# Performance work log

Measured on AMD Instinct MI355X. Metric: run time of the kernel, lower is better.

## Reference

```python
import jax, jax.numpy as jnp
import numpy as np

B, T, D, H, E = 16, 4096, 256, 512, 8


def setup_inputs() -> dict:
    key = jax.random.key(0)
    ks = jax.random.split(key, 5)
    x = jax.random.normal(ks[0], (B, T, D), dtype=jnp.float32)
    gate_w = jax.random.normal(ks[1], (D, E), dtype=jnp.float32) * 0.02
    gate_b = jnp.zeros((E,), dtype=jnp.float32)
    W1 = jax.random.normal(ks[2], (E, D, H), dtype=jnp.float32) * 0.02
    b1 = jnp.zeros((E, H), dtype=jnp.float32)
    W2 = jax.random.normal(ks[3], (E, H, D), dtype=jnp.float32) * 0.02
    b2 = jnp.zeros((E, D), dtype=jnp.float32)
    return {"x": x, "gate_w": gate_w, "gate_b": gate_b,
            "W1": W1, "b1": b1, "W2": W2, "b2": b2}


def reference(x, gate_w, gate_b, W1, b1, W2, b2):
    Bb, Tt, Dd = x.shape
    Ee = gate_w.shape[1]
    xf = x.reshape(-1, Dd)                       # [N, D]
    N = xf.shape[0]
    logits = xf @ gate_w + gate_b                # [N, E]
    probs = jax.nn.softmax(logits, axis=-1)
    top2_vals, top2_idx = jax.lax.top_k(probs, 2)  # [N, 2]
    # combine weights: w[n, e] = sum_k top2_vals[n,k] * (top2_idx[n,k]==e)
    cw = jnp.zeros((N, Ee), dtype=xf.dtype).at[
        jnp.arange(N)[:, None], top2_idx].add(top2_vals)  # [N, E]

    def step(acc, params):
        w1, bb1, w2, bb2, we = params            # per-expert slices
        h = jax.nn.gelu(xf @ w1 + bb1, approximate=False)  # [N, H]
        y = h @ w2 + bb2                          # [N, D]
        return acc + we[:, None] * y, None

    out, _ = jax.lax.scan(step, jnp.zeros_like(xf),
                          (W1, b1, W2, b2, cw.T))
    return out.reshape(Bb, Tt, Dd)
```

## Files before the change

### kernel.cpp

```cpp
#include <hip/hip_runtime.h>
#include <hip/hip_bf16.h>
#include <math.h>


#define N_TOK 65536
#define D_DIM 256
#define H_DIM 512
#define TILE_R 64
#define GRID_TILES 1088

typedef __bf16 bf16x8 __attribute__((ext_vector_type(8)));
typedef float f32x4 __attribute__((ext_vector_type(4)));

static __device__ __forceinline__ ushort f2bf(float f) {
    __hip_bfloat16 h = __float2bfloat16(f);
    ushort u;
    __builtin_memcpy(&u, &h, 2);
    return u;
}

static __device__ __forceinline__ float gelu(float v) {
    const float a = fabsf(v) * 0.70710678118654752f;
    const float t = __builtin_amdgcn_rcpf(fmaf(a, 0.47047f, 1.0f));
    const float p = t * fmaf(t, fmaf(t, 0.7478556f, -0.0958798f), 0.3480242f);
    const float er = fmaf(-p, __expf(-a * a), 1.0f);
    const float s = copysignf(er, v);
    return 0.5f * v * (1.0f + s);
}

__global__ __launch_bounds__(256) void prep(const float* __restrict__ x,
                                            const float* __restrict__ gate_w,
                                            const float* __restrict__ gate_b,
                                            const float* __restrict__ W1,
                                            const float* __restrict__ W2,
                                            ushort* __restrict__ xb,
                                            ushort* __restrict__ W1p,
                                            ushort* __restrict__ W2p,
                                            int* __restrict__ counts,
                                            int* __restrict__ pid_arr,
                                            float2* __restrict__ pw_arr) {
    __shared__ float gws[2048];
    __shared__ int lc[64];

    const int bid = blockIdx.x;
    const int tid = threadIdx.x;

    if (bid >= 2048) {
        const int pid = bid - 2048;
        const int t = (pid & 511) * 256 + tid;
        const int l = t & 63;
        const int lo = l & 15, hi = l >> 4;
        ushort v[8];
        if (pid < 512) {
            const int kb = (t >> 6) & 7;
            const int nb = (t >> 9) & 31;
            const int e  = t >> 14;
            const int k0 = kb * 32 + hi * 8;
            const int n  = nb * 16 + lo;
            const float* src = W1 + (size_t)e * D_DIM * H_DIM + n;
            #pragma unroll
            for (int j = 0; j < 8; ++j)
                v[j] = f2bf(src[(size_t)(k0 + j) * H_DIM]);
            *(uint4*)(W1p + (size_t)t * 8) = *(const uint4*)v;
        } else {
            const int kb = (t >> 6) & 15;
            const int nb = (t >> 10) & 15;
            const int e  = t >> 14;
            const int k0 = kb * 32 + hi * 8;
            const int n  = nb * 16 + lo;
            const float* src = W2 + (size_t)e * H_DIM * D_DIM + n;
            #pragma unroll
            for (int j = 0; j < 8; ++j)
                v[j] = f2bf(src[(size_t)(k0 + j) * D_DIM]);
            *(uint4*)(W2p + (size_t)t * 8) = *(const uint4*)v;
        }
        return;
    }

    const size_t t0 = (size_t)bid * 32;
    for (int i = tid; i < 2048; i += 256) gws[i] = gate_w[i];
    if (tid < 64) lc[tid] = 0;
    __syncthreads();

    const int m = tid >> 3, q = tid & 7;
    const float4* xr = (const float4*)(x + (t0 + m) * D_DIM + q * 32);
    ushort4* xw = (ushort4*)(xb + (t0 + m) * D_DIM + q * 32);

    double lg[8] = {0, 0, 0, 0, 0, 0, 0, 0};
    #pragma unroll
    for (int it = 0; it < 8; ++it) {
        const float4 v = xr[it];
        ushort4 bv;
        bv.x = f2bf(v.x); bv.y = f2bf(v.y); bv.z = f2bf(v.z); bv.w = f2bf(v.w);
        xw[it] = bv;
        const float* g = &gws[(q * 32 + it * 4) * 8];
        const float vv[4] = {v.x, v.y, v.z, v.w};
        #pragma unroll
        for (int j = 0; j < 4; ++j) {
            const double xv = (double)vv[j];
            #pragma unroll
            for (int e2 = 0; e2 < 8; ++e2) lg[e2] += xv * (double)g[j * 8 + e2];
        }
    }
    #pragma unroll
    for (int e2 = 0; e2 < 8; ++e2) {
        lg[e2] += __shfl_xor(lg[e2], 1, 64);
        lg[e2] += __shfl_xor(lg[e2], 2, 64);
        lg[e2] += __shfl_xor(lg[e2], 4, 64);
    }

    if (q == 0) {
        int e0 = 0, e1 = -1;
        #pragma unroll
        for (int e2 = 0; e2 < 8; ++e2) lg[e2] += (double)gate_b[e2];
        double b0 = -1e300, b1v = -1e300;
        #pragma unroll
        for (int e2 = 0; e2 < 8; ++e2)
            if (lg[e2] > b0) { b0 = lg[e2]; e0 = e2; }
        #pragma unroll
        for (int e2 = 0; e2 < 8; ++e2)
            if (e2 != e0 && lg[e2] > b1v) { b1v = lg[e2]; e1 = e2; }
        double s = 0;
        #pragma unroll
        for (int e2 = 0; e2 < 8; ++e2) s += exp(lg[e2] - b0);
        const float p0 = (float)(1.0 / s);
        const float p1 = (float)(exp(b1v - b0) / s);
        const int pid = e0 * 8 + e1;
        atomicAdd(&lc[pid], 1);
        const int tok = (int)t0 + m;
        pid_arr[tok] = pid;
        pw_arr[tok] = make_float2(p0, p1);
    }
    __syncthreads();
    if (tid < 64 && lc[tid]) atomicAdd(&counts[tid], lc[tid]);
}

__global__ __launch_bounds__(256) void scatter(const int* __restrict__ counts,
                                               const int* __restrict__ pid_arr,
                                               const float2* __restrict__ pw_arr,
                                               int* __restrict__ cursor,
                                               int* __restrict__ tok_list,
                                               float* __restrict__ w0l,
                                               float* __restrict__ w1l) {
    __shared__ int lcnt[64];
    __shared__ int lbase[64];
    const int tid = threadIdx.x;
    const int t = blockIdx.x * 256 + tid;
    if (tid < 64) lcnt[tid] = 0;
    __syncthreads();
    const int pid = pid_arr[t];
    const float2 pw = pw_arr[t];
    const int lpos = atomicAdd(&lcnt[pid], 1);
    __syncthreads();
    if (tid < 64) {
        int s = 0;
        for (int i = 0; i < tid; ++i) s += counts[i];
        const int mine = lcnt[tid];
        lbase[tid] = s + (mine ? atomicAdd(&cursor[tid], mine) : 0);
    }
    __syncthreads();
    const int pos = lbase[pid] + lpos;
    tok_list[pos] = t;
    w0l[pos] = pw.x;
    w1l[pos] = pw.y;
}

__global__ __launch_bounds__(512, 4) void moe_expert(const ushort* __restrict__ xb,
                                                     const ushort* __restrict__ W1p,
                                                     const ushort* __restrict__ W2p,
                                                     const float* __restrict__ b1,
                                                     const float* __restrict__ b2,
                                                     const int* __restrict__ counts,
                                                     const int* __restrict__ tok_list,
                                                     const float* __restrict__ w0l,
                                                     const float* __restrict__ w1l,
                                                     float* __restrict__ out) {
    __shared__ __align__(16) char Xs[TILE_R * 512];
    __shared__ __align__(16) char Hs[TILE_R * 512];
    __shared__ int   toks[TILE_R];
    __shared__ float wgt[2][TILE_R];

    int n = 0;
    for (int i = 0; i < 64; ++i) n += (counts[i] + 63) >> 6;
    const int qn = n >> 3, rn = n & 7;
    const int xc = blockIdx.x & 7, ix = blockIdx.x >> 3;
    if (ix >= qn + (xc < rn ? 1 : 0)) return;
    const int wg = xc * qn + min(xc, rn) + ix;

    int pid = -1, row0 = 0, nv = 0, gbase = 0;
    int st = 0, sc = 0;
    for (int i = 0; i < 64; ++i) {
        const int c = counts[i];
        const int nt = (c + 63) >> 6;
        if (pid < 0 && wg < st + nt) { pid = i; row0 = (wg - st) << 6; nv = min(TILE_R, c - row0); gbase = sc; }
        st += nt; sc += c;
    }
    const int ea = pid >> 3, eb = pid & 7;
    const int gidx = gbase + row0;

    const int tid = threadIdx.x;
    const int w = tid >> 6, l = tid & 63;
    const int lo = l & 15, hi = l >> 4;

    if (tid < TILE_R) {
        const bool vld = tid < nv;
        const int src = gidx + (vld ? tid : 0);
        toks[tid]   = tok_list[src];
        wgt[0][tid] = vld ? w0l[src] : 0.f;
        wgt[1][tid] = vld ? w1l[src] : 0.f;
    }

    {
        const int r = tid >> 3;
        const int tk = tok_list[gidx + min(r, nv - 1)];
        const char* src = (const char*)(xb + (size_t)tk * D_DIM) + (tid & 7) * 64;
        char* dst = Xs + r * 512;
        const int bo = (tid & 7) * 64, sw = (r & 7) << 4;
        #pragma unroll
        for (int c = 0; c < 4; ++c)
            *(uint4*)(dst + ((bo + c * 16) ^ sw)) = *(const uint4*)(src + c * 16);
    }
    __syncthreads();

    f32x4 acc2[4][2];
    #pragma unroll
    for (int mi = 0; mi < 4; ++mi)
        #pragma unroll
        for (int ni = 0; ni < 2; ++ni)
            acc2[mi][ni] = (f32x4){0.f, 0.f, 0.f, 0.f};

    #pragma unroll 1
    for (int phase = 0; phase < 4; ++phase) {
        const int ph = phase >> 1, ch = phase & 1;
        const int ew = ph ? eb : ea;

        const char* w1b = (const char*)W1p + (size_t)(ew * 32 + ch * 16 + w * 2) * 8192 + (size_t)l * 16;

        f32x4 acc1[2][4];
        #pragma unroll
        for (int nb = 0; nb < 2; ++nb)
            #pragma unroll
            for (int tb = 0; tb < 4; ++tb)
                acc1[nb][tb] = (f32x4){0.f, 0.f, 0.f, 0.f};

        bf16x8 wf[2][2];
        wf[0][0] = *(const bf16x8*)(w1b);
        wf[0][1] = *(const bf16x8*)(w1b + 8192);

        #pragma unroll
        for (int ks = 0; ks < 8; ++ks) {
            const int cb = ks & 1, nx = cb ^ 1;
            if (ks < 7) {
                wf[nx][0] = *(const bf16x8*)(w1b + (ks + 1) * 1024);
                wf[nx][1] = *(const bf16x8*)(w1b + 8192 + (ks + 1) * 1024);
            }
            #pragma unroll
            for (int tb = 0; tb < 4; ++tb) {
                const int slot = tb * 16 + lo;
                const bf16x8 xf = *(const bf16x8*)(Xs + slot * 512 +
                                  ((ks * 64 + hi * 16) ^ ((slot & 7) << 4)));
                __builtin_amdgcn_s_setprio(1);
                #pragma unroll
                for (int nb = 0; nb < 2; ++nb)
                    acc1[nb][tb] = __builtin_amdgcn_mfma_f32_16x16x32_bf16(wf[cb][nb], xf, acc1[nb][tb], 0, 0, 0);
                __builtin_amdgcn_s_setprio(0);
            }
        }

        #pragma unroll
        for (int nb = 0; nb < 2; ++nb) {
            const int hcE = (ch * 16 + w * 2 + nb) * 16 + hi * 4;
            const int hcH = (w * 2 + nb) * 16 + hi * 4;
            const float4 b1q = *(const float4*)(b1 + ew * H_DIM + hcE);
            #pragma unroll
            for (int tb = 0; tb < 4; ++tb) {
                const int slot = tb * 16 + lo;
                const float wt = wgt[ph][slot];
                ushort4 hv;
                hv.x = f2bf(gelu(acc1[nb][tb][0] + b1q.x) * wt);
                hv.y = f2bf(gelu(acc1[nb][tb][1] + b1q.y) * wt);
                hv.z = f2bf(gelu(acc1[nb][tb][2] + b1q.z) * wt);
                hv.w = f2bf(gelu(acc1[nb][tb][3] + b1q.w) * wt);
                *(ushort4*)(Hs + slot * 512 + ((hcH * 2) ^ ((slot & 7) << 4))) = hv;
            }
        }
        __syncthreads();

        const char* w2b = (const char*)W2p + ((size_t)(ew * 16 + w * 2) * 16 + ch * 8) * 1024 + (size_t)l * 16;

        bf16x8 wf2[3][2];
        #pragma unroll
        for (int p = 0; p < 2; ++p) {
            wf2[p][0] = *(const bf16x8*)(w2b + p * 1024);
            wf2[p][1] = *(const bf16x8*)(w2b + 16384 + p * 1024);
        }

        #pragma unroll
        for (int ks = 0; ks < 8; ++ks) {
            const int cb = ks % 3;
            if (ks < 6) {
                const int lb = (ks + 2) % 3;
                wf2[lb][0] = *(const bf16x8*)(w2b + (ks + 2) * 1024);
                wf2[lb][1] = *(const bf16x8*)(w2b + 16384 + (ks + 2) * 1024);
            }
            #pragma unroll
            for (int mi = 0; mi < 4; ++mi) {
                const int slot = mi * 16 + lo;
                const bf16x8 hf = *(const bf16x8*)(Hs + slot * 512 +
                                  ((ks * 64 + hi * 16) ^ ((slot & 7) << 4)));
                __builtin_amdgcn_s_setprio(1);
                #pragma unroll
                for (int ni = 0; ni < 2; ++ni)
                    acc2[mi][ni] = __builtin_amdgcn_mfma_f32_16x16x32_bf16(hf, wf2[cb][ni], acc2[mi][ni], 0, 0, 0);
                __builtin_amdgcn_s_setprio(0);
            }
        }
        if (phase < 3) __syncthreads();
    }

    #pragma unroll
    for (int ni = 0; ni < 2; ++ni) {
        const int col = w * 32 + ni * 16 + lo;
        const float b2a = b2[ea * D_DIM + col];
        const float b2b = b2[eb * D_DIM + col];
        #pragma unroll
        for (int mi = 0; mi < 4; ++mi) {
            #pragma unroll
            for (int rg = 0; rg < 4; ++rg) {
                const int r = mi * 16 + hi * 4 + rg;
                if (r < nv) {
                    const float v = acc2[mi][ni][rg] + wgt[0][r] * b2a + wgt[1][r] * b2b;
                    out[(size_t)toks[r] * D_DIM + col] = v;
                }
            }
        }
    }
}

extern "C" void kernel_launch(void* const* d_in, const int* in_sizes, int n_in,
                              void* d_out, int out_size, void* d_ws, size_t ws_size,
                              hipStream_t stream) {
    const float* x      = (const float*)d_in[0];
    const float* gate_w = (const float*)d_in[1];
    const float* gate_b = (const float*)d_in[2];
    const float* W1     = (const float*)d_in[3];
    const float* b1     = (const float*)d_in[4];
    const float* W2     = (const float*)d_in[5];
    const float* b2     = (const float*)d_in[6];
    float* out = (float*)d_out;

    char* ws = (char*)d_ws;
    ushort* xb      = (ushort*)(ws);
    ushort* W1p     = (ushort*)(ws + 33554432);
    ushort* W2p     = (ushort*)(ws + 35651584);
    int*    pid_arr = (int*)   (ws + 37748736);
    float2* pw_arr  = (float2*)(ws + 38010880);
    int*    tok_lst = (int*)   (ws + 38535168);
    float*  w0l     = (float*) (ws + 38797312);
    float*  w1l     = (float*) (ws + 39059456);
    int*    counts  = (int*)   (ws + 39321600);
    int*    cursor  = (int*)   (ws + 39321856);

    hipMemsetAsync(counts, 0, 512, stream);

    prep<<<dim3(3072), 256, 0, stream>>>(x, gate_w, gate_b, W1, W2,
                                         xb, W1p, W2p, counts, pid_arr, pw_arr);
    scatter<<<dim3(256), 256, 0, stream>>>(counts, pid_arr, pw_arr, cursor,
                                           tok_lst, w0l, w1l);
    moe_expert<<<dim3(GRID_TILES), 512, 0, stream>>>(xb, W1p, W2p, b1, b2, counts,
                                                     tok_lst, w0l, w1l, out);
}
```

Baseline: 199.9 us.

## Prefetch W1 fragments across phases with triple buffering and transpose gate weights

After: 185.7 us. 1.08x faster.

```diff
diff --git a/kernel.cpp b/kernel.cpp
--- a/kernel.cpp
+++ b/kernel.cpp
@@ -39,7 +39,7 @@
                                             int* __restrict__ counts,
                                             int* __restrict__ pid_arr,
                                             float2* __restrict__ pw_arr) {
-    __shared__ float gws[2048];
+    __shared__ float gwsT[8 * 260];
     __shared__ int lc[64];
 
     const int bid = blockIdx.x;
@@ -78,28 +78,32 @@
     }
 
     const size_t t0 = (size_t)bid * 32;
-    for (int i = tid; i < 2048; i += 256) gws[i] = gate_w[i];
+    for (int i = tid; i < 2048; i += 256) {
+        const int d = i >> 3, e = i & 7;
+        gwsT[e * 260 + d] = gate_w[i];
+    }
     if (tid < 64) lc[tid] = 0;
     __syncthreads();
 
     const int m = tid >> 3, q = tid & 7;
-    const float4* xr = (const float4*)(x + (t0 + m) * D_DIM + q * 32);
-    ushort4* xw = (ushort4*)(xb + (t0 + m) * D_DIM + q * 32);
+    const float* xrow = x + (t0 + m) * D_DIM;
+    ushort* xbrow = xb + (t0 + m) * D_DIM;
 
     double lg[8] = {0, 0, 0, 0, 0, 0, 0, 0};
     #pragma unroll
     for (int it = 0; it < 8; ++it) {
-        const float4 v = xr[it];
+        const int d0 = it * 32 + q * 4;
+        const float4 v = *(const float4*)(xrow + d0);
         ushort4 bv;
         bv.x = f2bf(v.x); bv.y = f2bf(v.y); bv.z = f2bf(v.z); bv.w = f2bf(v.w);
-        xw[it] = bv;
-        const float* g = &gws[(q * 32 + it * 4) * 8];
+        *(ushort4*)(xbrow + d0) = bv;
         const float vv[4] = {v.x, v.y, v.z, v.w};
         #pragma unroll
         for (int j = 0; j < 4; ++j) {
             const double xv = (double)vv[j];
             #pragma unroll
-            for (int e2 = 0; e2 < 8; ++e2) lg[e2] += xv * (double)g[j * 8 + e2];
+            for (int e2 = 0; e2 < 8; ++e2)
+                lg[e2] += xv * (double)gwsT[e2 * 260 + d0 + j];
         }
     }
     #pragma unroll
@@ -202,6 +206,13 @@
     const int w = tid >> 6, l = tid & 63;
     const int lo = l & 15, hi = l >> 4;
 
+    const char* w1b = (const char*)W1p + (size_t)(ea * 32 + w * 2) * 8192 + (size_t)l * 16;
+    bf16x8 wf[3][2];
+    wf[0][0] = *(const bf16x8*)(w1b);
+    wf[0][1] = *(const bf16x8*)(w1b + 8192);
+    wf[1][0] = *(const bf16x8*)(w1b + 1024);
+    wf[1][1] = *(const bf16x8*)(w1b + 8192 + 1024);
+
     if (tid < TILE_R) {
         const bool vld = tid < nv;
         const int src = gidx + (vld ? tid : 0);
@@ -234,8 +245,6 @@
         const int ph = phase >> 1, ch = phase & 1;
         const int ew = ph ? eb : ea;
 
-        const char* w1b = (const char*)W1p + (size_t)(ew * 32 + ch * 16 + w * 2) * 8192 + (size_t)l * 16;
-
         f32x4 acc1[2][4];
         #pragma unroll
         for (int nb = 0; nb < 2; ++nb)
@@ -243,16 +252,13 @@
             for (int tb = 0; tb < 4; ++tb)
                 acc1[nb][tb] = (f32x4){0.f, 0.f, 0.f, 0.f};
 
-        bf16x8 wf[2][2];
-        wf[0][0] = *(const bf16x8*)(w1b);
-        wf[0][1] = *(const bf16x8*)(w1b + 8192);
-
         #pragma unroll
         for (int ks = 0; ks < 8; ++ks) {
-            const int cb = ks & 1, nx = cb ^ 1;
-            if (ks < 7) {
-                wf[nx][0] = *(const bf16x8*)(w1b + (ks + 1) * 1024);
-                wf[nx][1] = *(const bf16x8*)(w1b + 8192 + (ks + 1) * 1024);
+            const int cb = ks % 3;
+            if (ks < 6) {
+                const int lb = (ks + 2) % 3;
+                wf[lb][0] = *(const bf16x8*)(w1b + (ks + 2) * 1024);
+                wf[lb][1] = *(const bf16x8*)(w1b + 8192 + (ks + 2) * 1024);
             }
             #pragma unroll
             for (int tb = 0; tb < 4; ++tb) {
@@ -284,16 +290,15 @@
                 *(ushort4*)(Hs + slot * 512 + ((hcH * 2) ^ ((slot & 7) << 4))) = hv;
             }
         }
-        __syncthreads();
 
         const char* w2b = (const char*)W2p + ((size_t)(ew * 16 + w * 2) * 16 + ch * 8) * 1024 + (size_t)l * 16;
-
         bf16x8 wf2[3][2];
         #pragma unroll
         for (int p = 0; p < 2; ++p) {
             wf2[p][0] = *(const bf16x8*)(w2b + p * 1024);
             wf2[p][1] = *(const bf16x8*)(w2b + 16384 + p * 1024);
         }
+        __syncthreads();
 
         #pragma unroll
         for (int ks = 0; ks < 8; ++ks) {
@@ -315,7 +320,18 @@
                 __builtin_amdgcn_s_setprio(0);
             }
         }
-        if (phase < 3) __syncthreads();
+
+        if (phase < 3) {
+            const int pn = phase + 1;
+            const int phn = pn >> 1, chn = pn & 1;
+            const int ewn = phn ? eb : ea;
+            w1b = (const char*)W1p + (size_t)(ewn * 32 + chn * 16 + w * 2) * 8192 + (size_t)l * 16;
+            wf[0][0] = *(const bf16x8*)(w1b);
+            wf[0][1] = *(const bf16x8*)(w1b + 8192);
+            wf[1][0] = *(const bf16x8*)(w1b + 1024);
+            wf[1][1] = *(const bf16x8*)(w1b + 8192 + 1024);
+            __syncthreads();
+        }
     }
 
     #pragma unroll
```
